# Performance work log

Measured on AMD Instinct MI355X. Metric: run time of the kernel, lower is better.

Reference implementation:

```python
import jax, jax.numpy as jnp
import numpy as np

N_NODES = 100000
N_EDGES = 20000
NNZ = 1600000


def _hconv(x, W, b, node_idx, edge_idx):
    # torch-geometric HypergraphConv, no attention, hyperedge_weight = 1
    x = x @ W                                                   # [N, F_out]
    ones = jnp.ones((NNZ,), dtype=x.dtype)
    deg_e = jax.ops.segment_sum(ones, edge_idx, num_segments=N_EDGES)   # |e|
    deg_n = jax.ops.segment_sum(ones, node_idx, num_segments=N_NODES)   # node degree
    B = jnp.where(deg_e > 0, 1.0 / deg_e, 0.0)
    D = jnp.where(deg_n > 0, 1.0 / deg_n, 0.0)
    # node -> edge: e_feat[e] = B_e * sum_{i in e} x_i
    e_feat = B[:, None] * jax.ops.segment_sum(x[node_idx], edge_idx, num_segments=N_EDGES)
    # edge -> node: out[i] = D_i * sum_{e ni i} e_feat[e]
    out = D[:, None] * jax.ops.segment_sum(e_feat[edge_idx], node_idx, num_segments=N_NODES)
    return out + b


def setup_inputs() -> dict:
    key = jax.random.key(0)
    ks = jax.random.split(key, 9)
    x = jax.random.normal(ks[0], (N_NODES, 128), dtype=jnp.float32)
    node_idx = jax.random.randint(ks[1], (NNZ,), 0, N_NODES, dtype=jnp.int64 if jax.config.jax_enable_x64 else jnp.int32)
    edge_idx = jax.random.randint(ks[2], (NNZ,), 0, N_EDGES, dtype=jnp.int64 if jax.config.jax_enable_x64 else jnp.int32)
    def lin(k, fi, fo):
        s = 1.0 / np.sqrt(fi)
        return jax.random.uniform(k, (fi, fo), jnp.float32, -s, s)
    W1 = lin(ks[3], 128, 128); b1 = jnp.zeros((128,), jnp.float32)
    W2 = lin(ks[4], 128, 128); b2 = jnp.zeros((128,), jnp.float32)
    W3 = lin(ks[5], 128, 64);  b3 = jnp.zeros((64,), jnp.float32)
    return {"x": x, "W1": W1, "b1": b1, "W2": W2, "b2": b2, "W3": W3, "b3": b3,
            "node_idx": node_idx, "edge_idx": edge_idx}


def reference(x, W1, b1, W2, b2, W3, b3, node_idx, edge_idx):
    h = _hconv(x, W1, b1, node_idx, edge_idx)
    h = jax.nn.relu(h)          # dropout p=0 -> identity
    h = _hconv(h, W2, b2, node_idx, edge_idx)
    h = jax.nn.relu(h)
    h = _hconv(h, W3, b3, node_idx, edge_idx)
    return h
```

## Files before the change

kernel.cpp:

```cpp
#include <hip/hip_runtime.h>

#define N_NODES 100000
#define N_EDGES 20000
#define NNZV    1600000
#define NSEG    (N_EDGES + N_NODES)
#define FIN     128
#define HSLICES 64
#define SLICE   (NNZV / HSLICES)
#define NR_E    4
#define NR_N    16
#define NRANGES (NR_E + NR_N)

__device__ __forceinline__ unsigned short f2bf(float f) {
  unsigned u = __float_as_uint(f);
  unsigned r = u + 0x7fffu + ((u >> 16) & 1u);
  return (unsigned short)(r >> 16);
}
__device__ __forceinline__ unsigned pack2(float lo, float hi) {
  return (unsigned)f2bf(lo) | ((unsigned)f2bf(hi) << 16);
}
__device__ __forceinline__ float bf_lo(unsigned w) { return __uint_as_float(w << 16); }
__device__ __forceinline__ float bf_hi(unsigned w) { return __uint_as_float(w & 0xffff0000u); }

__device__ __forceinline__ void range_info(int r, const int* nidx, const int* eidx,
                                           const int*& keys, const int*& vals,
                                           int& base, int& size, int& gbin_off) {
  if (r < NR_E) { keys = eidx; vals = nidx; base = r * 5000; size = 5000; gbin_off = 0; }
  else { keys = nidx; vals = eidx; base = (r - NR_E) * 6250; size = 6250; gbin_off = N_EDGES; }
}


__global__ __launch_bounds__(256) void k_hist(const int* __restrict__ nidx,
                                              const int* __restrict__ eidx,
                                              int* __restrict__ part) {
  __shared__ int hist[6250];
  int r = blockIdx.x % NRANGES, s = blockIdx.x / NRANGES;
  const int *keys, *vals; int base, size, gbin_off;
  range_info(r, nidx, eidx, keys, vals, base, size, gbin_off);
  for (int i = threadIdx.x; i < size; i += 256) hist[i] = 0;
  __syncthreads();
  int lo = s * SLICE, hi = lo + SLICE;
  for (int i = lo + threadIdx.x; i < hi; i += 256) {
    int k = keys[i];
    unsigned d = (unsigned)(k - base);
    if (d < (unsigned)size) atomicAdd(&hist[d], 1);
  }
  __syncthreads();
  int* dst = part + (size_t)s * NSEG + gbin_off + base;
  for (int i = threadIdx.x; i < size; i += 256) dst[i] = hist[i];
}

__global__ void k_hreduce(const int* __restrict__ part, int* __restrict__ cnt) {
  int b = blockIdx.x * 256 + threadIdx.x;
  if (b >= NSEG) return;
  int sum = 0;
  for (int s = 0; s < HSLICES; ++s) sum += part[(size_t)s * NSEG + b];
  cnt[b] = sum;
}


__global__ void k_scan1(const int* __restrict__ cnt, int* __restrict__ incl,
                        int* __restrict__ bsum) {
  __shared__ int s[1024];
  int gid = blockIdx.x * 1024 + threadIdx.x;
  int v = (gid < NSEG) ? cnt[gid] : 0;
  s[threadIdx.x] = v;
  __syncthreads();
  for (int d = 1; d < 1024; d <<= 1) {
    int t = (threadIdx.x >= d) ? s[threadIdx.x - d] : 0;
    __syncthreads();
    s[threadIdx.x] += t;
    __syncthreads();
  }
  if (gid < NSEG) incl[gid] = s[threadIdx.x];
  if (threadIdx.x == 1023) bsum[blockIdx.x] = s[1023];
}

__global__ void k_scan2(int* __restrict__ bsum, int nb) {
  __shared__ int s[128];
  int v = (threadIdx.x < nb) ? bsum[threadIdx.x] : 0;
  s[threadIdx.x] = v;
  __syncthreads();
  for (int d = 1; d < 128; d <<= 1) {
    int t = (threadIdx.x >= (unsigned)d) ? s[threadIdx.x - d] : 0;
    __syncthreads();
    s[threadIdx.x] += t;
    __syncthreads();
  }
  if (threadIdx.x < nb) bsum[threadIdx.x] = s[threadIdx.x] - v;
}

__global__ void k_scan3(int* __restrict__ off, const int* __restrict__ cnt,
                        const int* __restrict__ bsum) {
  int gid = blockIdx.x * 1024 + threadIdx.x;
  if (gid < NSEG) off[gid] = off[gid] - cnt[gid] + bsum[blockIdx.x];
}


__global__ void k_sbase(int* __restrict__ part, const int* __restrict__ off) {
  int b = blockIdx.x * 256 + threadIdx.x;
  if (b >= NSEG) return;
  int running = off[b];
  for (int s = 0; s < HSLICES; ++s) {
    size_t idx = (size_t)s * NSEG + b;
    int t = part[idx];
    part[idx] = running;
    running += t;
  }
}


__global__ __launch_bounds__(256) void k_fill3(const int* __restrict__ nidx,
                                               const int* __restrict__ eidx,
                                               const int* __restrict__ sbase,
                                               int* __restrict__ csr) {
  __shared__ int rank[6250];
  int r = blockIdx.x % NRANGES, s = blockIdx.x / NRANGES;
  const int *keys, *vals; int base, size, gbin_off;
  range_info(r, nidx, eidx, keys, vals, base, size, gbin_off);
  for (int i = threadIdx.x; i < size; i += 256) rank[i] = 0;
  __syncthreads();
  int lo = s * SLICE, hi = lo + SLICE;
  const int* sb = sbase + (size_t)s * NSEG + gbin_off;
  for (int i = lo + threadIdx.x; i < hi; i += 256) {
    int k = keys[i];
    unsigned d = (unsigned)(k - base);
    if (d < (unsigned)size) {
      int v = vals[i];
      int rk = atomicAdd(&rank[d], 1);
      csr[sb[k] + rk] = v;
    }
  }
}


__global__ void k_tobf(const float2* __restrict__ x2, unsigned* __restrict__ xbf) {
  int t = blockIdx.x * 256 + threadIdx.x;
  float2 v = x2[t];
  xbf[t] = pack2(v.x, v.y);
}


__global__ __launch_bounds__(256) void k_passAbf(const unsigned* __restrict__ tab,
                                                 const int* __restrict__ csr,
                                                 const int* __restrict__ off,
                                                 const int* __restrict__ cnt,
                                                 float* __restrict__ ebuf) {
  int wave = (blockIdx.x * blockDim.x + threadIdx.x) >> 6;
  int lane = threadIdx.x & 63;
  if (wave >= N_EDGES) return;
  int beg = off[wave];
  int m   = cnt[wave];
  const unsigned* src = tab + lane;
  float accx = 0.f, accy = 0.f;
  int idxv = 0;
  int j = 0;
  for (; j + 8 <= m; j += 8) {
    int jm = j & 63;
    if (jm == 0) {
      int p = j + lane;
      idxv = (p < m) ? __builtin_nontemporal_load(csr + beg + p) : 0;
    }
    int n0 = __shfl(idxv, jm);
    int n1 = __shfl(idxv, jm + 1);
    int n2 = __shfl(idxv, jm + 2);
    int n3 = __shfl(idxv, jm + 3);
    int n4 = __shfl(idxv, jm + 4);
    int n5 = __shfl(idxv, jm + 5);
    int n6 = __shfl(idxv, jm + 6);
    int n7 = __shfl(idxv, jm + 7);
    unsigned w0 = src[(size_t)n0 * 64];
    unsigned w1 = src[(size_t)n1 * 64];
    unsigned w2 = src[(size_t)n2 * 64];
    unsigned w3 = src[(size_t)n3 * 64];
    unsigned w4 = src[(size_t)n4 * 64];
    unsigned w5 = src[(size_t)n5 * 64];
    unsigned w6 = src[(size_t)n6 * 64];
    unsigned w7 = src[(size_t)n7 * 64];
    accx += ((bf_lo(w0) + bf_lo(w1)) + (bf_lo(w2) + bf_lo(w3))) +
            ((bf_lo(w4) + bf_lo(w5)) + (bf_lo(w6) + bf_lo(w7)));
    accy += ((bf_hi(w0) + bf_hi(w1)) + (bf_hi(w2) + bf_hi(w3))) +
            ((bf_hi(w4) + bf_hi(w5)) + (bf_hi(w6) + bf_hi(w7)));
  }
  for (; j < m; ++j) {
    int jm = j & 63;
    if (jm == 0) {
      int p = j + lane;
      idxv = (p < m) ? __builtin_nontemporal_load(csr + beg + p) : 0;
    }
    int n0 = __shfl(idxv, jm);
    unsigned w = src[(size_t)n0 * 64];
    accx += bf_lo(w); accy += bf_hi(w);
  }
  float binv = (m > 0) ? (1.f / (float)m) : 0.f;
  *reinterpret_cast<float2*>(ebuf + (size_t)wave * FIN + lane * 2) =
      make_float2(accx * binv, accy * binv);
}


__global__ void k_gemm128b(const float* __restrict__ A, const float* __restrict__ W,
                           unsigned* __restrict__ Out) {
  __shared__ float As[64][33];
  __shared__ float Ws[32][128];
  int tid = threadIdx.x;
  int tx = tid % 16, ty = tid / 16;
  int row0 = blockIdx.x * 64;
  float acc[4][8];
#pragma unroll
  for (int i = 0; i < 4; ++i)
#pragma unroll
    for (int j = 0; j < 8; ++j) acc[i][j] = 0.f;

  for (int kc = 0; kc < FIN; kc += 32) {
    for (int i = tid; i < 64 * 32; i += 256) {
      int r = i >> 5, k = i & 31;
      int gr = row0 + r;
      As[r][k] = (gr < N_EDGES) ? A[(size_t)gr * FIN + kc + k] : 0.f;
    }
    for (int i = tid; i < 32 * 128; i += 256) {
      int k = i >> 7, cc = i & 127;
      Ws[k][cc] = W[(size_t)(kc + k) * 128 + cc];
    }
    __syncthreads();
#pragma unroll
    for (int k = 0; k < 32; ++k) {
      float a[4];
#pragma unroll
      for (int i = 0; i < 4; ++i) a[i] = As[ty * 4 + i][k];
      float w[8];
#pragma unroll
      for (int j = 0; j < 8; ++j) w[j] = Ws[k][tx * 8 + j];
#pragma unroll
      for (int i = 0; i < 4; ++i)
#pragma unroll
        for (int j = 0; j < 8; ++j) acc[i][j] += a[i] * w[j];
    }
    __syncthreads();
  }
#pragma unroll
  for (int i = 0; i < 4; ++i) {
    int gr = row0 + ty * 4 + i;
    if (gr < N_EDGES) {
#pragma unroll
      for (int jj = 0; jj < 4; ++jj)
        Out[(size_t)gr * 64 + tx * 4 + jj] = pack2(acc[i][2 * jj], acc[i][2 * jj + 1]);
    }
  }
}


template <bool RELU>
__global__ __launch_bounds__(256) void k_passBbf(const unsigned* __restrict__ tab,
                                                 const int* __restrict__ csr,
                                                 const int* __restrict__ off,
                                                 const int* __restrict__ cnt,
                                                 const float* __restrict__ bias,
                                                 unsigned* __restrict__ hbf) {
  int wave = (blockIdx.x * blockDim.x + threadIdx.x) >> 6;
  int lane = threadIdx.x & 63;
  if (wave >= N_NODES) return;
  int beg = off[N_EDGES + wave];
  int m   = cnt[N_EDGES + wave];
  const unsigned* src = tab + lane;
  float accx = 0.f, accy = 0.f;
  int idxv = 0;
  int j = 0;
  for (; j + 8 <= m; j += 8) {
    int jm = j & 63;
    if (jm == 0) {
      int p = j + lane;
      idxv = (p < m) ? __builtin_nontemporal_load(csr + beg + p) : 0;
    }
    int n0 = __shfl(idxv, jm);
    int n1 = __shfl(idxv, jm + 1);
    int n2 = __shfl(idxv, jm + 2);
    int n3 = __shfl(idxv, jm + 3);
    int n4 = __shfl(idxv, jm + 4);
    int n5 = __shfl(idxv, jm + 5);
    int n6 = __shfl(idxv, jm + 6);
    int n7 = __shfl(idxv, jm + 7);
    unsigned w0 = src[(size_t)n0 * 64];
    unsigned w1 = src[(size_t)n1 * 64];
    unsigned w2 = src[(size_t)n2 * 64];
    unsigned w3 = src[(size_t)n3 * 64];
    unsigned w4 = src[(size_t)n4 * 64];
    unsigned w5 = src[(size_t)n5 * 64];
    unsigned w6 = src[(size_t)n6 * 64];
    unsigned w7 = src[(size_t)n7 * 64];
    accx += ((bf_lo(w0) + bf_lo(w1)) + (bf_lo(w2) + bf_lo(w3))) +
            ((bf_lo(w4) + bf_lo(w5)) + (bf_lo(w6) + bf_lo(w7)));
    accy += ((bf_hi(w0) + bf_hi(w1)) + (bf_hi(w2) + bf_hi(w3))) +
            ((bf_hi(w4) + bf_hi(w5)) + (bf_hi(w6) + bf_hi(w7)));
  }
  for (; j < m; ++j) {
    int jm = j & 63;
    if (jm == 0) {
      int p = j + lane;
      idxv = (p < m) ? __builtin_nontemporal_load(csr + beg + p) : 0;
    }
    int n0 = __shfl(idxv, jm);
    unsigned w = src[(size_t)n0 * 64];
    accx += bf_lo(w); accy += bf_hi(w);
  }
  float dinv = (m > 0) ? (1.f / (float)m) : 0.f;
  float ox = accx * dinv + bias[lane * 2];
  float oy = accy * dinv + bias[lane * 2 + 1];
  if (RELU) { ox = fmaxf(ox, 0.f); oy = fmaxf(oy, 0.f); }
  hbf[(size_t)wave * 64 + lane] = pack2(ox, oy);
}


__global__ void k_gemm_node_b(const unsigned* __restrict__ hbf, const float* __restrict__ W,
                              unsigned* __restrict__ Out) {
  __shared__ float As[64][33];
  __shared__ float Ws[32][64];
  int tid = threadIdx.x;
  int tx = tid % 8, ty = tid / 8;
  int row0 = blockIdx.x * 64;
  float acc[4][8];
#pragma unroll
  for (int i = 0; i < 4; ++i)
#pragma unroll
    for (int j = 0; j < 8; ++j) acc[i][j] = 0.f;

  for (int kc = 0; kc < FIN; kc += 32) {
    for (int i = tid; i < 64 * 16; i += 128) {
      int r = i >> 4, kp = i & 15;
      int gr = row0 + r;
      unsigned w = (gr < N_NODES) ? hbf[(size_t)gr * 64 + (kc >> 1) + kp] : 0u;
      As[r][2 * kp]     = bf_lo(w);
      As[r][2 * kp + 1] = bf_hi(w);
    }
    for (int i = tid; i < 32 * 64; i += 128) {
      int k = i >> 6, cc = i & 63;
      Ws[k][cc] = W[(size_t)(kc + k) * 64 + cc];
    }
    __syncthreads();
#pragma unroll
    for (int k = 0; k < 32; ++k) {
      float a[4];
#pragma unroll
      for (int i = 0; i < 4; ++i) a[i] = As[ty * 4 + i][k];
      float w[8];
#pragma unroll
      for (int j = 0; j < 8; ++j) w[j] = Ws[k][tx * 8 + j];
#pragma unroll
      for (int i = 0; i < 4; ++i)
#pragma unroll
        for (int j = 0; j < 8; ++j) acc[i][j] += a[i] * w[j];
    }
    __syncthreads();
  }
#pragma unroll
  for (int i = 0; i < 4; ++i) {
    int gr = row0 + ty * 4 + i;
    if (gr < N_NODES) {
#pragma unroll
      for (int jj = 0; jj < 4; ++jj)
        Out[(size_t)gr * 32 + tx * 4 + jj] = pack2(acc[i][2 * jj], acc[i][2 * jj + 1]);
    }
  }
}


__global__ __launch_bounds__(256) void k_passA64b(const unsigned short* __restrict__ tab,
                                                  const int* __restrict__ csr,
                                                  const int* __restrict__ off,
                                                  const int* __restrict__ cnt,
                                                  unsigned short* __restrict__ eb3) {
  int wave = (blockIdx.x * blockDim.x + threadIdx.x) >> 6;
  int lane = threadIdx.x & 63;
  if (wave >= N_EDGES) return;
  int beg = off[wave];
  int m   = cnt[wave];
  const unsigned short* src = tab + lane;
  float acc = 0.f;
  int idxv = 0;
  int j = 0;
  for (; j + 8 <= m; j += 8) {
    int jm = j & 63;
    if (jm == 0) {
      int p = j + lane;
      idxv = (p < m) ? __builtin_nontemporal_load(csr + beg + p) : 0;
    }
    int n0 = __shfl(idxv, jm);
    int n1 = __shfl(idxv, jm + 1);
    int n2 = __shfl(idxv, jm + 2);
    int n3 = __shfl(idxv, jm + 3);
    int n4 = __shfl(idxv, jm + 4);
    int n5 = __shfl(idxv, jm + 5);
    int n6 = __shfl(idxv, jm + 6);
    int n7 = __shfl(idxv, jm + 7);
    float v0 = __uint_as_float((unsigned)src[(size_t)n0 * 64] << 16);
    float v1 = __uint_as_float((unsigned)src[(size_t)n1 * 64] << 16);
    float v2 = __uint_as_float((unsigned)src[(size_t)n2 * 64] << 16);
    float v3 = __uint_as_float((unsigned)src[(size_t)n3 * 64] << 16);
    float v4 = __uint_as_float((unsigned)src[(size_t)n4 * 64] << 16);
    float v5 = __uint_as_float((unsigned)src[(size_t)n5 * 64] << 16);
    float v6 = __uint_as_float((unsigned)src[(size_t)n6 * 64] << 16);
    float v7 = __uint_as_float((unsigned)src[(size_t)n7 * 64] << 16);
    acc += ((v0 + v1) + (v2 + v3)) + ((v4 + v5) + (v6 + v7));
  }
  for (; j < m; ++j) {
    int jm = j & 63;
    if (jm == 0) {
      int p = j + lane;
      idxv = (p < m) ? __builtin_nontemporal_load(csr + beg + p) : 0;
    }
    int n0 = __shfl(idxv, jm);
    acc += __uint_as_float((unsigned)src[(size_t)n0 * 64] << 16);
  }
  float binv = (m > 0) ? (1.f / (float)m) : 0.f;
  eb3[(size_t)wave * 64 + lane] = f2bf(acc * binv);
}


__global__ __launch_bounds__(256) void k_passB64b(const unsigned short* __restrict__ tab,
                                                  const int* __restrict__ csr,
                                                  const int* __restrict__ off,
                                                  const int* __restrict__ cnt,
                                                  const float* __restrict__ bias,
                                                  float* __restrict__ out) {
  int wave = (blockIdx.x * blockDim.x + threadIdx.x) >> 6;
  int lane = threadIdx.x & 63;
  if (wave >= N_NODES) return;
  int beg = off[N_EDGES + wave];
  int m   = cnt[N_EDGES + wave];
  const unsigned short* src = tab + lane;
  float acc = 0.f;
  int idxv = 0;
  int j = 0;
  for (; j + 8 <= m; j += 8) {
    int jm = j & 63;
    if (jm == 0) {
      int p = j + lane;
      idxv = (p < m) ? __builtin_nontemporal_load(csr + beg + p) : 0;
    }
    int n0 = __shfl(idxv, jm);
    int n1 = __shfl(idxv, jm + 1);
    int n2 = __shfl(idxv, jm + 2);
    int n3 = __shfl(idxv, jm + 3);
    int n4 = __shfl(idxv, jm + 4);
    int n5 = __shfl(idxv, jm + 5);
    int n6 = __shfl(idxv, jm + 6);
    int n7 = __shfl(idxv, jm + 7);
    float v0 = __uint_as_float((unsigned)src[(size_t)n0 * 64] << 16);
    float v1 = __uint_as_float((unsigned)src[(size_t)n1 * 64] << 16);
    float v2 = __uint_as_float((unsigned)src[(size_t)n2 * 64] << 16);
    float v3 = __uint_as_float((unsigned)src[(size_t)n3 * 64] << 16);
    float v4 = __uint_as_float((unsigned)src[(size_t)n4 * 64] << 16);
    float v5 = __uint_as_float((unsigned)src[(size_t)n5 * 64] << 16);
    float v6 = __uint_as_float((unsigned)src[(size_t)n6 * 64] << 16);
    float v7 = __uint_as_float((unsigned)src[(size_t)n7 * 64] << 16);
    acc += ((v0 + v1) + (v2 + v3)) + ((v4 + v5) + (v6 + v7));
  }
  for (; j < m; ++j) {
    int jm = j & 63;
    if (jm == 0) {
      int p = j + lane;
      idxv = (p < m) ? __builtin_nontemporal_load(csr + beg + p) : 0;
    }
    int n0 = __shfl(idxv, jm);
    acc += __uint_as_float((unsigned)src[(size_t)n0 * 64] << 16);
  }
  float dinv = (m > 0) ? (1.f / (float)m) : 0.f;
  out[(size_t)wave * 64 + lane] = acc * dinv + bias[lane];
}


extern "C" void kernel_launch(void* const* d_in, const int* in_sizes, int n_in,
                              void* d_out, int out_size, void* d_ws, size_t ws_size,
                              hipStream_t stream) {
  const float* x  = (const float*)d_in[0];
  const float* W1 = (const float*)d_in[1];
  const float* b1 = (const float*)d_in[2];
  const float* W2 = (const float*)d_in[3];
  const float* b2 = (const float*)d_in[4];
  const float* W3 = (const float*)d_in[5];
  const float* b3 = (const float*)d_in[6];
  const int* nidx = (const int*)d_in[7];
  const int* eidx = (const int*)d_in[8];

  const size_t OFF_CNT  = 0;
  const size_t OFF_OFF  = 480000;
  const size_t OFF_BSUM = 1440000;
  const size_t OFF_CSR  = 1441792;
  const size_t OFF_EB   = 14241792;
  const size_t OFF_EB2  = 24481792;
  const size_t OFF_XBF  = 29601792;
  const size_t OFF_HBF  = 55201792;
  const size_t NEEDED   = 80801792;
  if (ws_size < NEEDED) return;

  char* ws = (char*)d_ws;
  int*      cnt   = (int*)(ws + OFF_CNT);
  int*      off   = (int*)(ws + OFF_OFF);
  int*      bsum  = (int*)(ws + OFF_BSUM);
  int*      csr   = (int*)(ws + OFF_CSR);
  int*      part  = (int*)(ws + OFF_XBF);
  float*    ebuf  = (float*)(ws + OFF_EB);
  unsigned* eb2bf = (unsigned*)(ws + OFF_EB2);
  unsigned* xbf   = (unsigned*)(ws + OFF_XBF);
  unsigned* hw3   = (unsigned*)(ws + OFF_XBF);
  unsigned short* eb3 = (unsigned short*)(ws + OFF_EB);
  unsigned* hbf   = (unsigned*)(ws + OFF_HBF);
  float*    out   = (float*)d_out;

  hipMemsetAsync(ws + OFF_BSUM, 0, 512, stream);

  k_hist<<<NRANGES * HSLICES, 256, 0, stream>>>(nidx, eidx, part);
  k_hreduce<<<(NSEG + 255) / 256, 256, 0, stream>>>(part, cnt);
  const int nb = (NSEG + 1023) / 1024;
  k_scan1<<<nb, 1024, 0, stream>>>(cnt, off, bsum);
  k_scan2<<<1, 128, 0, stream>>>(bsum, nb);
  k_scan3<<<nb, 1024, 0, stream>>>(off, cnt, bsum);
  k_sbase<<<(NSEG + 255) / 256, 256, 0, stream>>>(part, off);
  k_fill3<<<NRANGES * HSLICES, 256, 0, stream>>>(nidx, eidx, part, csr);

  k_tobf<<<25000, 256, 0, stream>>>((const float2*)x, xbf);

  const int BLK_A = (N_EDGES * 64 + 255) / 256;
  const int BLK_B = (N_NODES * 64 + 255) / 256;
  const int BLK_G = (N_EDGES + 63) / 64;
  const int BLK_GN = (N_NODES + 63) / 64;

  k_passAbf<<<BLK_A, 256, 0, stream>>>(xbf, csr, off, cnt, ebuf);
  k_gemm128b<<<BLK_G, 256, 0, stream>>>(ebuf, W1, eb2bf);
  k_passBbf<true><<<BLK_B, 256, 0, stream>>>(eb2bf, csr, off, cnt, b1, hbf);

  k_passAbf<<<BLK_A, 256, 0, stream>>>(hbf, csr, off, cnt, ebuf);
  k_gemm128b<<<BLK_G, 256, 0, stream>>>(ebuf, W2, eb2bf);
  k_passBbf<true><<<BLK_B, 256, 0, stream>>>(eb2bf, csr, off, cnt, b2, hbf);

  k_gemm_node_b<<<BLK_GN, 128, 0, stream>>>(hbf, W3, hw3);
  k_passA64b<<<BLK_A, 256, 0, stream>>>((const unsigned short*)hw3, csr, off, cnt, eb3);
  k_passB64b<<<BLK_B, 256, 0, stream>>>(eb3, csr, off, cnt, b3, out);
}
```

Baseline: 611.2 us.

## Store edge aggregates as bf16 and remap fill blocks across XCDs

Pass A now writes the per-edge mean features packed as bf16 pairs rather than fp32, and the edge GEMM reads the packed bf16 operand and unpacks it in registers. This halves the traffic for the intermediate edge buffer. Separately, the CSR fill kernel splits the edge key range into 8 smaller ranges (24 total) and maps block IDs so that each XCD handles a consistent range, aiming for better L2 locality and less shared-memory atomic contention. It trades some precision in the intermediate edge features and launches more fill blocks, each of which rescans its input slice.

```diff
diff --git a/kernel.cpp b/kernel.cpp
--- a/kernel.cpp
+++ b/kernel.cpp
@@ -23,10 +23,9 @@
 __device__ __forceinline__ float bf_hi(unsigned w) { return __uint_as_float(w & 0xffff0000u); }
 
 __device__ __forceinline__ void range_info(int r, const int* nidx, const int* eidx,
-                                           const int*& keys, const int*& vals,
-                                           int& base, int& size, int& gbin_off) {
-  if (r < NR_E) { keys = eidx; vals = nidx; base = r * 5000; size = 5000; gbin_off = 0; }
-  else { keys = nidx; vals = eidx; base = (r - NR_E) * 6250; size = 6250; gbin_off = N_EDGES; }
+                                           const int*& keys, int& base, int& size, int& gbin_off) {
+  if (r < NR_E) { keys = eidx; base = r * 5000; size = 5000; gbin_off = 0; }
+  else { keys = nidx; base = (r - NR_E) * 6250; size = 6250; gbin_off = N_EDGES; }
 }
 
 
@@ -35,8 +34,8 @@
                                               int* __restrict__ part) {
   __shared__ int hist[6250];
   int r = blockIdx.x % NRANGES, s = blockIdx.x / NRANGES;
-  const int *keys, *vals; int base, size, gbin_off;
-  range_info(r, nidx, eidx, keys, vals, base, size, gbin_off);
+  const int* keys; int base, size, gbin_off;
+  range_info(r, nidx, eidx, keys, base, size, gbin_off);
   for (int i = threadIdx.x; i < size; i += 256) hist[i] = 0;
   __syncthreads();
   int lo = s * SLICE, hi = lo + SLICE;
@@ -115,9 +114,15 @@
                                                const int* __restrict__ sbase,
                                                int* __restrict__ csr) {
   __shared__ int rank[6250];
-  int r = blockIdx.x % NRANGES, s = blockIdx.x / NRANGES;
+  int g = blockIdx.x;
+  int xcd = g & 7;
+  int i2 = g >> 3;
+  int li = i2 % 3;
+  int s  = i2 / 3;
+  int r  = li * 8 + xcd;
   const int *keys, *vals; int base, size, gbin_off;
-  range_info(r, nidx, eidx, keys, vals, base, size, gbin_off);
+  if (r < 8) { keys = eidx; vals = nidx; base = r * 2500; size = 2500; gbin_off = 0; }
+  else { keys = nidx; vals = eidx; base = (r - 8) * 6250; size = 6250; gbin_off = N_EDGES; }
   for (int i = threadIdx.x; i < size; i += 256) rank[i] = 0;
   __syncthreads();
   int lo = s * SLICE, hi = lo + SLICE;
@@ -145,7 +150,7 @@
                                                  const int* __restrict__ csr,
                                                  const int* __restrict__ off,
                                                  const int* __restrict__ cnt,
-                                                 float* __restrict__ ebuf) {
+                                                 unsigned* __restrict__ ebuf) {
   int wave = (blockIdx.x * blockDim.x + threadIdx.x) >> 6;
   int lane = threadIdx.x & 63;
   if (wave >= N_EDGES) return;
@@ -193,14 +198,14 @@
     accx += bf_lo(w); accy += bf_hi(w);
   }
   float binv = (m > 0) ? (1.f / (float)m) : 0.f;
-  *reinterpret_cast<float2*>(ebuf + (size_t)wave * FIN + lane * 2) =
-      make_float2(accx * binv, accy * binv);
-}
-
-
-__global__ void k_gemm128b(const float* __restrict__ A, const float* __restrict__ W,
-                           unsigned* __restrict__ Out) {
-  __shared__ float As[64][33];
+  ebuf[(size_t)wave * 64 + lane] = pack2(accx * binv, accy * binv);
+}
+
+
+__global__ __launch_bounds__(256) void k_gemm128b(const unsigned* __restrict__ Abf,
+                                                  const float* __restrict__ W,
+                                                  unsigned* __restrict__ Out) {
+  __shared__ unsigned Asp[64][17];
   __shared__ float Ws[32][128];
   int tid = threadIdx.x;
   int tx = tid % 16, ty = tid / 16;
@@ -212,10 +217,10 @@
     for (int j = 0; j < 8; ++j) acc[i][j] = 0.f;
 
   for (int kc = 0; kc < FIN; kc += 32) {
-    for (int i = tid; i < 64 * 32; i += 256) {
-      int r = i >> 5, k = i & 31;
+    for (int i = tid; i < 64 * 16; i += 256) {
+      int r = i >> 4, kp = i & 15;
       int gr = row0 + r;
-      As[r][k] = (gr < N_EDGES) ? A[(size_t)gr * FIN + kc + k] : 0.f;
+      Asp[r][kp] = (gr < N_EDGES) ? Abf[(size_t)gr * 64 + (kc >> 1) + kp] : 0u;
     }
     for (int i = tid; i < 32 * 128; i += 256) {
       int k = i >> 7, cc = i & 127;
@@ -223,17 +228,24 @@
     }
     __syncthreads();
 #pragma unroll
-    for (int k = 0; k < 32; ++k) {
-      float a[4];
-#pragma unroll
-      for (int i = 0; i < 4; ++i) a[i] = As[ty * 4 + i][k];
-      float w[8];
-#pragma unroll
-      for (int j = 0; j < 8; ++j) w[j] = Ws[k][tx * 8 + j];
+    for (int kp = 0; kp < 16; ++kp) {
+      float alo[4], ahi[4];
+#pragma unroll
+      for (int i = 0; i < 4; ++i) {
+        unsigned w = Asp[ty * 4 + i][kp];
+        alo[i] = bf_lo(w); ahi[i] = bf_hi(w);
+      }
+      float w0[8], w1[8];
+#pragma unroll
+      for (int j = 0; j < 8; ++j) {
+        w0[j] = Ws[2 * kp][tx * 8 + j];
+        w1[j] = Ws[2 * kp + 1][tx * 8 + j];
+      }
 #pragma unroll
       for (int i = 0; i < 4; ++i)
 #pragma unroll
-        for (int j = 0; j < 8; ++j) acc[i][j] += a[i] * w[j];
+        for (int j = 0; j < 8; ++j)
+          acc[i][j] += alo[i] * w0[j] + ahi[i] * w1[j];
     }
     __syncthreads();
   }
@@ -498,7 +510,7 @@
   int*      bsum  = (int*)(ws + OFF_BSUM);
   int*      csr   = (int*)(ws + OFF_CSR);
   int*      part  = (int*)(ws + OFF_XBF);
-  float*    ebuf  = (float*)(ws + OFF_EB);
+  unsigned* ebuf  = (unsigned*)(ws + OFF_EB);
   unsigned* eb2bf = (unsigned*)(ws + OFF_EB2);
   unsigned* xbf   = (unsigned*)(ws + OFF_XBF);
   unsigned* hw3   = (unsigned*)(ws + OFF_XBF);
@@ -515,7 +527,7 @@
   k_scan2<<<1, 128, 0, stream>>>(bsum, nb);
   k_scan3<<<nb, 1024, 0, stream>>>(off, cnt, bsum);
   k_sbase<<<(NSEG + 255) / 256, 256, 0, stream>>>(part, off);
-  k_fill3<<<NRANGES * HSLICES, 256, 0, stream>>>(nidx, eidx, part, csr);
+  k_fill3<<<24 * HSLICES, 256, 0, stream>>>(nidx, eidx, part, csr);
 
   k_tobf<<<25000, 256, 0, stream>>>((const float2*)x, xbf);
 
```

After: 620.1 us. Within noise of the previous version (+1.5%).
